# Optimization experiments

Measured on AMD Instinct MI355X. Metric: run time of the kernel, lower is better.

The kernel has to match this reference:

```python
import jax, jax.numpy as jnp
import numpy as np

NUM_GROUPS = 32
EPS = 1e-5


def _conv(x, w, b, pad):
    # x: [B,C,H,W], w: [O,I,kh,kw]
    y = jax.lax.conv_general_dilated(
        x, w, window_strides=(1, 1), padding=[(pad, pad), (pad, pad)],
        dimension_numbers=('NCHW', 'OIHW', 'NCHW'))
    return y + b[None, :, None, None]


def _group_norm(x, gamma, beta):
    B, C, H, W = x.shape
    g = x.reshape(B, NUM_GROUPS, C // NUM_GROUPS, H, W)
    mu = g.mean(axis=(2, 3, 4), keepdims=True)
    var = g.var(axis=(2, 3, 4), keepdims=True)
    g = (g - mu) * jax.lax.rsqrt(var + EPS)
    x = g.reshape(B, C, H, W)
    return x * gamma[None, :, None, None] + beta[None, :, None, None]


def setup_inputs() -> dict:
    key = jax.random.key(0)
    ks = jax.random.split(key, 8)
    B, C, H, W = 8, 384, 64, 64
    s1 = 1.0 / np.sqrt(C)          # 1x1 conv fan-in
    s3 = 1.0 / np.sqrt(C * 9)      # 3x3 conv fan-in
    return {
        'x': jax.random.normal(ks[0], (B, C, H, W), dtype=jnp.float32),
        'gamma': jnp.ones((C,), dtype=jnp.float32),
        'beta': jnp.zeros((C,), dtype=jnp.float32),
        'wq': jax.random.normal(ks[1], (C, C, 1, 1), dtype=jnp.float32) * s1,
        'bq': jnp.zeros((C,), dtype=jnp.float32),
        'wk': jax.random.normal(ks[2], (C, C, 3, 3), dtype=jnp.float32) * s3,
        'bk': jnp.zeros((C,), dtype=jnp.float32),
        'wv': jax.random.normal(ks[3], (C, C, 1, 1), dtype=jnp.float32) * s1,
        'bv': jnp.zeros((C,), dtype=jnp.float32),
        'wf': jax.random.normal(ks[4], (C, C, 1, 1), dtype=jnp.float32) * s1,
        'bf': jnp.zeros((C,), dtype=jnp.float32),
        'k': 512,
    }


def reference(x, gamma, beta, wq, bq, wk, bk, wv, bv, wf, bf, k):
    B, C, H, W = x.shape
    xn = _group_norm(x, gamma, beta)
    q = _conv(xn, wq, bq, 0)
    kk = _conv(xn, wk, bk, 1)
    v = _conv(xn, wv, bv, 0)
    # frequency-domain correlation: elementwise product of 2D spectra
    Fq = jnp.fft.fft2(q)
    Fk = jnp.fft.fft2(kk)
    A = jnp.fft.ifft2(Fq * Fk).real          # [B,C,H,W]
    # per-(batch,channel) spatial top-k sparsification
    A_flat = A.reshape(B, C, H * W)
    topv, _ = jax.lax.top_k(A_flat, k)
    thresh = topv[..., -1:]                   # k-th largest value
    masked = jnp.where(A_flat >= thresh, A_flat, -jnp.inf)
    Fw = jax.nn.softmax(masked, axis=-1).reshape(B, C, H, W)
    F4 = v * Fw                               # weighted values
    res = _conv(F4, wf, bf, 0)
    return xn * res
```

## Files before the change

### kernel.cpp

```cpp
#include <hip/hip_runtime.h>
#include <hip/hip_fp16.h>
#include <math.h>

#define CCH  384
#define BATCH 8
#define HWN  4096
#define NG   32
#define CPG  12
#define KSEL 512
#define FFTP 65
#define LP   40

typedef short v8s  __attribute__((ext_vector_type(8)));
typedef float v16f __attribute__((ext_vector_type(16)));

#define MFMA_B16(A_,B_,C_) __builtin_amdgcn_mfma_f32_32x32x16_bf16((A_),(B_),(C_),0,0,0)

#define BARRIER_NODRAIN() asm volatile("s_waitcnt lgkmcnt(0)\n\ts_barrier" ::: "memory")

__device__ __forceinline__ v8s as_v8s(uint4 u) {
  union { uint4 u4; v8s v; } c; c.u4 = u; return c.v;
}
__device__ __forceinline__ unsigned br6(unsigned i) {
  return ((i&1u)<<5)|((i&2u)<<3)|((i&4u)<<1)|((i&8u)>>1)|((i&16u)>>3)|((i&32u)>>5);
}
__device__ __forceinline__ unsigned f2key(float f) {
  unsigned u = __float_as_uint(f);
  return (u & 0x80000000u) ? ~u : (u | 0x80000000u);
}
__device__ __forceinline__ float wave_max(float v) {
#pragma unroll
  for (int o = 32; o > 0; o >>= 1) v = fmaxf(v, __shfl_down(v, o, 64));
  return v;
}
__device__ __forceinline__ float wave_sum(float v) {
#pragma unroll
  for (int o = 32; o > 0; o >>= 1) v += __shfl_down(v, o, 64);
  return v;
}
__device__ __forceinline__ unsigned short bf16_rne(float f) {
  unsigned u = __float_as_uint(f);
  return (unsigned short)((u + 0x7fffu + ((u >> 16) & 1u)) >> 16);
}
__device__ __forceinline__ float bf2f(unsigned short h) {
  return __uint_as_float(((unsigned)h) << 16);
}

__global__ __launch_bounds__(256) void stats_kernel(const float* __restrict__ x,
                                                    float2* __restrict__ gs) {
  int b = blockIdx.x >> 5, g = blockIdx.x & 31;
  size_t base = ((size_t)b * CCH + (size_t)g * CPG) * HWN;
  const float4* xp = (const float4*)(x + base);
  int tid = threadIdx.x;
  const int N4 = CPG * HWN / 4;
  float s = 0.f, ss = 0.f;
  for (int i = tid; i < N4; i += 256) {
    float4 v = xp[i];
    s  += (v.x + v.y) + (v.z + v.w);
    ss += (v.x*v.x + v.y*v.y) + (v.z*v.z + v.w*v.w);
  }
  s = wave_sum(s); ss = wave_sum(ss);
  __shared__ float sb[4], qb[4];
  if ((tid & 63) == 0) { sb[tid >> 6] = s; qb[tid >> 6] = ss; }
  __syncthreads();
  if (tid == 0) {
    float S = sb[0]+sb[1]+sb[2]+sb[3], Q = qb[0]+qb[1]+qb[2]+qb[3];
    float inv = 1.0f / (float)(CPG * HWN);
    float mu = S * inv;
    float var = Q * inv - mu * mu;
    gs[blockIdx.x] = make_float2(mu, rsqrtf(var + 1e-5f));
  }
}

__global__ __launch_bounds__(256) void pack_split_k(const float* __restrict__ w,
    unsigned short* __restrict__ hi, unsigned short* __restrict__ lo, int n) {
  int i = blockIdx.x * 256 + threadIdx.x;
  if (i >= n) return;
  float f = w[i];
  int m = i / 384, ci = i - m * 384;
  int kc = ci >> 4, tt = ci & 15;
  int mb = m >> 5, lm2 = m & 31;
  int l = ((tt >> 3) << 5) | lm2;
  int j = tt & 7;
  size_t o = (((size_t)kc * 12 + mb) << 9) + ((size_t)l << 3) + j;
  unsigned short h = bf16_rne(f);
  hi[o] = h;
  lo[o] = bf16_rne(f - bf2f(h));
}
__global__ __launch_bounds__(256) void pack9_k(const float* __restrict__ w,
    unsigned short* __restrict__ hi, unsigned short* __restrict__ lo) {
  int i = blockIdx.x * 256 + threadIdx.x;
  int r = blockIdx.y;
  float f = w[(size_t)i * 9 + r];
  int m = i / 384, ci = i - m * 384;
  int kc = ci >> 4, tt = ci & 15;
  int mb = m >> 5, lm2 = m & 31;
  int l = ((tt >> 3) << 5) | lm2;
  int j = tt & 7;
  size_t o = (((size_t)(r * 24 + kc) * 12 + mb) << 9) + ((size_t)l << 3) + j;
  unsigned short h = bf16_rne(f);
  hi[o] = h;
  lo[o] = bf16_rne(f - bf2f(h));
}

template<int FUSE, int SPLIT>
__global__ __launch_bounds__(256) void trans_kernel(const float* __restrict__ in,
    const float2* __restrict__ gs, const float* __restrict__ gamma,
    const float* __restrict__ beta,
    unsigned short* __restrict__ oh, unsigned short* __restrict__ ol) {
  __shared__ float ts[64][65];
  int tid = threadIdx.x;
  int b = blockIdx.z, c0 = blockIdx.y * 64, p0 = blockIdx.x * 64;
#pragma unroll
  for (int i = 0; i < 4; ++i) {
    int idx = tid + (i << 8);
    int row = idx >> 4, col = (idx & 15) << 2;
    float4 v = *(const float4*)&in[((size_t)b*CCH + c0 + row)*HWN + p0 + col];
    if (FUSE) {
      int c = c0 + row;
      float2 st = gs[(b << 5) + c / CPG];
      float a = gamma[c] * st.y, bb = beta[c] - st.x * a;
      v.x = v.x*a+bb; v.y = v.y*a+bb; v.z = v.z*a+bb; v.w = v.w*a+bb;
    }
    ts[row][col] = v.x; ts[row][col+1] = v.y; ts[row][col+2] = v.z; ts[row][col+3] = v.w;
  }
  __syncthreads();
#pragma unroll
  for (int i = 0; i < 2; ++i) {
    int idx = tid + (i << 8);
    int p = idx >> 3, cgp = (idx & 7) << 3;
    unsigned short h8[8] __attribute__((aligned(16)));
    unsigned short l8[8] __attribute__((aligned(16)));
#pragma unroll
    for (int j = 0; j < 8; ++j) {
      float f = ts[cgp + j][p];
      unsigned short hb = bf16_rne(f);
      h8[j] = hb;
      if (SPLIT) l8[j] = bf16_rne(f - bf2f(hb));
    }
    size_t o = ((size_t)b*HWN + p0 + p)*CCH + c0 + cgp;
    *(uint4*)&oh[o] = *(const uint4*)h8;
    if (SPLIT) *(uint4*)&ol[o] = *(const uint4*)l8;
  }
}

template<int TAPS, int OUT>
__global__ __launch_bounds__(256, 3) void mm_kernel(
    const unsigned short* __restrict__ Ahg, const unsigned short* __restrict__ Alg,
    const float* __restrict__ bias,
    const unsigned short* __restrict__ Bhg, const unsigned short* __restrict__ Blg,
    const unsigned short* __restrict__ xnTh, const unsigned short* __restrict__ xnTl,
    void* __restrict__ Yv) {
  __shared__ unsigned short Bh_s[2][128*LP], Bl_s[2][128*LP];
  int tid = threadIdx.x;
  int b = blockIdx.z, m0 = blockIdx.y * 128, n0 = blockIdx.x * 128;
  int y0 = blockIdx.x * 2;
  int u0row = tid >> 2, cg = tid & 3;
  int lds0 = u0row * LP + cg * 8, lds1 = lds0 + 64 * LP;
  int lane = tid & 63, wm = tid >> 7, wn = (tid >> 6) & 1;
  int lm = lane & 31, lh = lane >> 5;
  int brow = (wn * 64 + lm) * LP;
  int mbb = blockIdx.y * 4 + wm * 2;
  int laneoff = lane << 3;

  v16f acc[2][2];
#pragma unroll
  for (int t = 0; t < 2; ++t)
#pragma unroll
    for (int s = 0; s < 2; ++s)
#pragma unroll
      for (int g = 0; g < 16; ++g) acc[t][s][g] = 0.f;

  const int NS = TAPS * 12;
  uint4 rb0h, rb0l, rb1h, rb1l;
  uint4 rA0h_h0, rA0l_h0, rA1h_h0, rA1l_h0;
  uint4 rA0h_h1, rA0l_h1, rA1h_h1, rA1l_h1;

  auto issueB = [&](int s) {
    int r  = (TAPS == 9) ? (s / 12) : 0;
    int c0 = (s - r * 12) * 32;
    int dy = (TAPS == 9) ? r / 3 - 1 : 0;
    int dx = (TAPS == 9) ? r % 3 - 1 : 0;
    int px = u0row + dx;
    int py0 = y0 + dy, py1 = py0 + 1;
    bool okx = (unsigned)px < 64u;
    bool ok0 = okx && ((unsigned)py0 < 64u);
    bool ok1 = okx && ((unsigned)py1 < 64u);
    size_t boff0 = ((size_t)b * HWN + py0 * 64 + px) * CCH + cg * 8 + c0;
    size_t boff1 = ((size_t)b * HWN + py1 * 64 + px) * CCH + cg * 8 + c0;
    uint4 zf; zf.x = zf.y = zf.z = zf.w = 0u;
    rb0h = ok0 ? *(const uint4*)(Bhg + boff0) : zf;
    rb0l = ok0 ? *(const uint4*)(Blg + boff0) : zf;
    rb1h = ok1 ? *(const uint4*)(Bhg + boff1) : zf;
    rb1l = ok1 ? *(const uint4*)(Blg + boff1) : zf;
  };
  auto loadA0 = [&](int s) {
    int fragcol;
    if (TAPS == 9) { int r = s / 12; fragcol = r * 24 + (s - r * 12) * 2; }
    else fragcol = s * 2;
    size_t off = (((size_t)fragcol * 12 + mbb) << 9) + laneoff;
    rA0h_h0 = *(const uint4*)(Ahg + off);
    rA0l_h0 = *(const uint4*)(Alg + off);
    rA1h_h0 = *(const uint4*)(Ahg + off + 512);
    rA1l_h0 = *(const uint4*)(Alg + off + 512);
  };
  auto loadA1 = [&](int s) {
    int fragcol;
    if (TAPS == 9) { int r = s / 12; fragcol = r * 24 + (s - r * 12) * 2 + 1; }
    else fragcol = s * 2 + 1;
    size_t off = (((size_t)fragcol * 12 + mbb) << 9) + laneoff;
    rA0h_h1 = *(const uint4*)(Ahg + off);
    rA0l_h1 = *(const uint4*)(Alg + off);
    rA1h_h1 = *(const uint4*)(Ahg + off + 512);
    rA1l_h1 = *(const uint4*)(Alg + off + 512);
  };

  issueB(0);
  loadA0(0); loadA1(0);
  *(uint4*)&Bh_s[0][lds0] = rb0h; *(uint4*)&Bl_s[0][lds0] = rb0l;
  *(uint4*)&Bh_s[0][lds1] = rb1h; *(uint4*)&Bl_s[0][lds1] = rb1l;
  issueB(1);
  BARRIER_NODRAIN();

  for (int s = 0; s < NS; ++s) {
    const int cur = s & 1;
    const unsigned short* Bh = &Bh_s[cur][0];
    const unsigned short* Bl = &Bl_s[cur][0];
    {
      int co = lh << 3;
      v8s b0h = *(const v8s*)&Bh[brow + co];
      v8s b0l = *(const v8s*)&Bl[brow + co];
      v8s b1h = *(const v8s*)&Bh[brow + 32*LP + co];
      v8s b1l = *(const v8s*)&Bl[brow + 32*LP + co];
      v8s a0h = as_v8s(rA0h_h0), a0l = as_v8s(rA0l_h0);
      v8s a1h = as_v8s(rA1h_h0), a1l = as_v8s(rA1l_h0);
      __builtin_amdgcn_s_setprio(1);
      acc[0][0] = MFMA_B16(a0h, b0h, acc[0][0]);
      acc[0][0] = MFMA_B16(a0h, b0l, acc[0][0]);
      acc[0][0] = MFMA_B16(a0l, b0h, acc[0][0]);
      acc[0][1] = MFMA_B16(a0h, b1h, acc[0][1]);
      acc[0][1] = MFMA_B16(a0h, b1l, acc[0][1]);
      acc[0][1] = MFMA_B16(a0l, b1h, acc[0][1]);
      acc[1][0] = MFMA_B16(a1h, b0h, acc[1][0]);
      acc[1][0] = MFMA_B16(a1h, b0l, acc[1][0]);
      acc[1][0] = MFMA_B16(a1l, b0h, acc[1][0]);
      acc[1][1] = MFMA_B16(a1h, b1h, acc[1][1]);
      acc[1][1] = MFMA_B16(a1h, b1l, acc[1][1]);
      acc[1][1] = MFMA_B16(a1l, b1h, acc[1][1]);
      __builtin_amdgcn_s_setprio(0);
    }
    if (s + 1 < NS) loadA0(s + 1);
    {
      int co = 16 + (lh << 3);
      v8s b0h = *(const v8s*)&Bh[brow + co];
      v8s b0l = *(const v8s*)&Bl[brow + co];
      v8s b1h = *(const v8s*)&Bh[brow + 32*LP + co];
      v8s b1l = *(const v8s*)&Bl[brow + 32*LP + co];
      v8s a0h = as_v8s(rA0h_h1), a0l = as_v8s(rA0l_h1);
      v8s a1h = as_v8s(rA1h_h1), a1l = as_v8s(rA1l_h1);
      __builtin_amdgcn_s_setprio(1);
      acc[0][0] = MFMA_B16(a0h, b0h, acc[0][0]);
      acc[0][0] = MFMA_B16(a0h, b0l, acc[0][0]);
      acc[0][0] = MFMA_B16(a0l, b0h, acc[0][0]);
      acc[0][1] = MFMA_B16(a0h, b1h, acc[0][1]);
      acc[0][1] = MFMA_B16(a0h, b1l, acc[0][1]);
      acc[0][1] = MFMA_B16(a0l, b1h, acc[0][1]);
      acc[1][0] = MFMA_B16(a1h, b0h, acc[1][0]);
      acc[1][0] = MFMA_B16(a1h, b0l, acc[1][0]);
      acc[1][0] = MFMA_B16(a1l, b0h, acc[1][0]);
      acc[1][1] = MFMA_B16(a1h, b1h, acc[1][1]);
      acc[1][1] = MFMA_B16(a1h, b1l, acc[1][1]);
      acc[1][1] = MFMA_B16(a1l, b1h, acc[1][1]);
      __builtin_amdgcn_s_setprio(0);
    }
    if (s + 1 < NS) {
      loadA1(s + 1);
      int nxt = cur ^ 1;
      *(uint4*)&Bh_s[nxt][lds0] = rb0h; *(uint4*)&Bl_s[nxt][lds0] = rb0l;
      *(uint4*)&Bh_s[nxt][lds1] = rb1h; *(uint4*)&Bl_s[nxt][lds1] = rb1l;
      if (s + 2 < NS) issueB(s + 2);
      BARRIER_NODRAIN();
    }
  }
#pragma unroll
  for (int t = 0; t < 2; ++t) {
    int mb = m0 + wm * 64 + t * 32;
#pragma unroll
    for (int s = 0; s < 2; ++s) {
      int n = n0 + wn * 64 + s * 32 + lm;
#pragma unroll
      for (int g = 0; g < 16; ++g) {
        int m = mb + (g & 3) + ((g >> 2) << 3) + (lh << 2);
        float val = acc[t][s][g] + bias[m];
        size_t oidx = ((size_t)b * CCH + m) * HWN + n;
        if (OUT == 0) {
          ((float*)Yv)[oidx] = val;
        } else if (OUT == 1) {
          ((__half*)Yv)[oidx] = __float2half(val);
        } else {
          size_t tix = ((size_t)b * HWN + n) * CCH + m;
          float xnv = bf2f(xnTh[tix]) + bf2f(xnTl[tix]);
          ((float*)Yv)[oidx] = val * xnv;
        }
      }
    }
  }
}

__device__ __forceinline__ void fft4_pass(float* zr, float* zi,
    const float* twr, const float* twi, int tid, int axis, float ds) {
#pragma unroll
  for (int s = 0; s < 3; ++s) {
    const int h = 1 << (2 * s);
#pragma unroll
    for (int tt = 0; tt < 4; ++tt) {
      int t = tid + (tt << 8);
      int line = t >> 4, bf = t & 15;
      int j  = bf & (h - 1);
      int i0 = ((bf >> (2 * s)) << (2 * s + 2)) + j;
      int e1 = j << (5 - 2 * s);
      int e2 = j << (4 - 2 * s);
      float w1r = twr[e1], w1i = ds * twi[e1];
      float w2r = twr[e2], w2i = ds * twi[e2];
      int A0, st;
      if (axis == 0) { A0 = line * FFTP + i0; st = h; }
      else           { A0 = i0 * FFTP + line; st = h * FFTP; }
      int A1 = A0 + st, A2 = A1 + st, A3 = A2 + st;
      float x0r = zr[A0], x0i = zi[A0];
      float x1r = zr[A1], x1i = zi[A1];
      float x2r = zr[A2], x2i = zi[A2];
      float x3r = zr[A3], x3i = zi[A3];
      float t1r = x1r*w1r - x1i*w1i, t1i = x1r*w1i + x1i*w1r;
      float t3r = x3r*w1r - x3i*w1i, t3i = x3r*w1i + x3i*w1r;
      float u0r = x0r + t1r, u0i = x0i + t1i;
      float u1r = x0r - t1r, u1i = x0i - t1i;
      float u2r = x2r + t3r, u2i = x2i + t3i;
      float u3r = x2r - t3r, u3i = x2i - t3i;
      float c2r = u2r*w2r - u2i*w2i, c2i = u2r*w2i + u2i*w2r;
      float c3r = u3r*w2r - u3i*w2i, c3i = u3r*w2i + u3i*w2r;
      zr[A0] = u0r + c2r;      zi[A0] = u0i + c2i;
      zr[A2] = u0r - c2r;      zi[A2] = u0i - c2i;
      zr[A1] = u1r + ds*c3i;   zi[A1] = u1i - ds*c3r;
      zr[A3] = u1r - ds*c3i;   zi[A3] = u1i + ds*c3r;
    }
    __syncthreads();
  }
}

__global__ __launch_bounds__(256) void fft_topk_kernel(
    const float* q, const float* __restrict__ kkb,
    const __half* __restrict__ v, float* F4) {
  __shared__ float zr[64 * FFTP], zi[64 * FFTP];
  __shared__ float twr[32], twi[32];
  __shared__ unsigned hist[256];
  __shared__ unsigned su2[2];
  __shared__ unsigned wtot[4];
  __shared__ float sred[5];
  int tid = threadIdx.x;
  int lane = tid & 63, w = tid >> 6;
  size_t base = (size_t)blockIdx.x * HWN;
  for (int i = tid; i < HWN; i += 256) {
    int y = i >> 6, x = i & 63;
    int slot = br6(y) * FFTP + br6(x);
    zr[slot] = q[base + i];
    zi[slot] = kkb[base + i];
  }
  if (tid < 32) {
    float ang = (float)tid * 0.0981747704246810387f;
    twr[tid] = cosf(ang);
    twi[tid] = -sinf(ang);
  }
  __syncthreads();
  fft4_pass(zr, zi, twr, twi, tid, 0, 1.f);
  fft4_pass(zr, zi, twr, twi, tid, 1, 1.f);
  float prr[16], pir[16];
#pragma unroll
  for (int c = 0; c < 16; c++) {
    int i = tid + (c << 8);
    int ky = i >> 6, kx = i & 63;
    float sr = zr[ky * FFTP + kx], si = zi[ky * FFTP + kx];
    int kyn = (64 - ky) & 63, kxn = (64 - kx) & 63;
    float nr = zr[kyn * FFTP + kxn], ni = zi[kyn * FFTP + kxn];
    float fqr = 0.5f * (sr + nr), fqi = 0.5f * (si - ni);
    float fkr = 0.5f * (si + ni), fki = 0.5f * (nr - sr);
    prr[c] = fqr * fkr - fqi * fki;
    pir[c] = fqr * fki + fqi * fkr;
  }
  __syncthreads();
#pragma unroll
  for (int c = 0; c < 16; c++) {
    int i = tid + (c << 8);
    int ky = i >> 6, kx = i & 63;
    int slot = br6(ky) * FFTP + br6(kx);
    zr[slot] = prr[c];
    zi[slot] = pir[c];
  }
  __syncthreads();
  fft4_pass(zr, zi, twr, twi, tid, 0, -1.f);
  fft4_pass(zr, zi, twr, twi, tid, 1, -1.f);
  const float scale = 1.0f / 4096.0f;
  float a[16];
  unsigned key[16];
  float mx = -3.0e38f;
#pragma unroll
  for (int c = 0; c < 16; c++) {
    int i = tid + (c << 8);
    a[c] = zr[(i >> 6) * FFTP + (i & 63)] * scale;
    key[c] = f2key(a[c]);
    mx = fmaxf(mx, a[c]);
  }
  mx = wave_max(mx);
  if (lane == 0) sred[w] = mx;
  __syncthreads();
  if (tid == 0) sred[4] = fmaxf(fmaxf(sred[0], sred[1]), fmaxf(sred[2], sred[3]));
  __syncthreads();
  float am = sred[4];
  unsigned prefix = 0; int kr = KSEL;
  for (int pass = 0; pass < 4; pass++) {
    int shift = 24 - (pass << 3);
    hist[tid] = 0;
    __syncthreads();
#pragma unroll
    for (int c = 0; c < 16; c++) {
      unsigned u = key[c];
      if (((u ^ prefix) >> shift) <= 0xFFu)
        atomicAdd(&hist[(u >> shift) & 255u], 1u);
    }
    __syncthreads();
    unsigned xv = hist[tid];
#pragma unroll
    for (int o = 1; o < 64; o <<= 1) {
      unsigned t2 = __shfl_down(xv, o, 64);
      if (lane + o < 64) xv += t2;
    }
    if (lane == 0) wtot[w] = xv;
    __syncthreads();
    for (int ww = w + 1; ww < 4; ++ww) xv += wtot[ww];
    hist[tid] = xv;
    __syncthreads();
    unsigned sv = xv;
    unsigned svn = (tid < 255) ? hist[tid + 1] : 0u;
    if (sv >= (unsigned)kr && svn < (unsigned)kr) { su2[0] = (unsigned)tid; su2[1] = svn; }
    __syncthreads();
    prefix |= su2[0] << shift;
    kr -= (int)su2[1];
  }
  unsigned thr = prefix;
  float lsum = 0.f;
#pragma unroll
  for (int c = 0; c < 16; c++)
    if (key[c] >= thr) lsum += expf(a[c] - am);
  lsum = wave_sum(lsum);
  if (lane == 0) sred[w] = lsum;
  __syncthreads();
  if (tid == 0) sred[4] = 1.0f / (sred[0] + sred[1] + sred[2] + sred[3]);
  __syncthreads();
  float inv = sred[4];
#pragma unroll
  for (int c = 0; c < 16; c++) {
    int i = tid + (c << 8);
    float wgt = (key[c] >= thr) ? expf(a[c] - am) * inv : 0.f;
    F4[base + i] = __half2float(v[base + i]) * wgt;
  }
}

extern "C" void kernel_launch(void* const* d_in, const int* in_sizes, int n_in,
                              void* d_out, int out_size, void* d_ws, size_t ws_size,
                              hipStream_t stream) {
  const float* x     = (const float*)d_in[0];
  const float* gamma = (const float*)d_in[1];
  const float* beta  = (const float*)d_in[2];
  const float* wq    = (const float*)d_in[3];
  const float* bq    = (const float*)d_in[4];
  const float* wk    = (const float*)d_in[5];
  const float* bk    = (const float*)d_in[6];
  const float* wv    = (const float*)d_in[7];
  const float* bv    = (const float*)d_in[8];
  const float* wf    = (const float*)d_in[9];
  const float* bf    = (const float*)d_in[10];

  const size_t NEL = (size_t)BATCH * CCH * HWN;
  const size_t WSZ = (size_t)CCH * CCH;

  unsigned short* xnTh = (unsigned short*)d_ws;
  unsigned short* xnTl = xnTh + NEL;
  float*  qC  = (float*)(xnTl + NEL);
  float*  kD  = qC + NEL;
  __half* vE  = (__half*)(kD + NEL);
  unsigned short* W = (unsigned short*)(vE + NEL);
  unsigned short* Wqh = W;
  unsigned short* Wql = Wqh + WSZ;
  unsigned short* Wvh = Wql + WSZ;
  unsigned short* Wvl = Wvh + WSZ;
  unsigned short* Wfh = Wvl + WSZ;
  unsigned short* Wfl = Wfh + WSZ;
  unsigned short* Wkh = Wfl + WSZ;
  unsigned short* Wkl = Wkh + 9 * WSZ;
  float2* gs = (float2*)(Wkl + 9 * WSZ);
  unsigned short* F4Th = (unsigned short*)kD;
  unsigned short* F4Tl = F4Th + NEL;

  pack_split_k<<<dim3(576), dim3(256), 0, stream>>>(wq, Wqh, Wql, (int)WSZ);
  pack_split_k<<<dim3(576), dim3(256), 0, stream>>>(wv, Wvh, Wvl, (int)WSZ);
  pack_split_k<<<dim3(576), dim3(256), 0, stream>>>(wf, Wfh, Wfl, (int)WSZ);
  pack9_k<<<dim3(576, 9), dim3(256), 0, stream>>>(wk, Wkh, Wkl);
  stats_kernel<<<dim3(BATCH * NG), dim3(256), 0, stream>>>(x, gs);
  trans_kernel<1, 1><<<dim3(64, 6, BATCH), dim3(256), 0, stream>>>(
      x, gs, gamma, beta, xnTh, xnTl);

  dim3 gm(32, 3, BATCH);
  mm_kernel<1, 0><<<gm, dim3(256), 0, stream>>>(Wqh, Wql, bq, xnTh, xnTl,
                                                nullptr, nullptr, qC);
  mm_kernel<9, 0><<<gm, dim3(256), 0, stream>>>(Wkh, Wkl, bk, xnTh, xnTl,
                                                nullptr, nullptr, kD);
  mm_kernel<1, 1><<<gm, dim3(256), 0, stream>>>(Wvh, Wvl, bv, xnTh, xnTl,
                                                nullptr, nullptr, vE);

  fft_topk_kernel<<<dim3(BATCH * CCH), dim3(256), 0, stream>>>(qC, kD, vE, qC);

  trans_kernel<0, 1><<<dim3(64, 6, BATCH), dim3(256), 0, stream>>>(
      qC, nullptr, nullptr, nullptr, F4Th, F4Tl);

  mm_kernel<1, 2><<<gm, dim3(256), 0, stream>>>(Wfh, Wfl, bf, F4Th, F4Tl,
                                                xnTh, xnTl, d_out);
}
```

Baseline: 669.1 us.

## Stream GEMM B tiles directly into swizzled LDS with global_load_lds

The B operand of the bf16-split GEMM now goes straight from global memory into LDS with global_load_lds, instead of passing through registers and then being stored to LDS. The padded LDS rows are replaced by an XOR-swizzled 32-element layout to avoid bank conflicts. Out-of-bounds taps read from a small zeroed buffer, which stats_kernel clears. The main loop is reordered to one barrier per stage, independent MFMAs are interleaved, and launch bounds rise to 4 blocks per CU. This frees VGPRs and cuts LDS store traffic, but it relies on the async LDS writes being complete at a bare s_barrier with no explicit wait. It also places the zero buffer after gs, which may lie outside the allocated workspace.

```diff
diff --git a/kernel.cpp b/kernel.cpp
--- a/kernel.cpp
+++ b/kernel.cpp
@@ -9,14 +9,19 @@
 #define CPG  12
 #define KSEL 512
 #define FFTP 65
-#define LP   40
 
 typedef short v8s  __attribute__((ext_vector_type(8)));
 typedef float v16f __attribute__((ext_vector_type(16)));
 
 #define MFMA_B16(A_,B_,C_) __builtin_amdgcn_mfma_f32_32x32x16_bf16((A_),(B_),(C_),0,0,0)
 
-#define BARRIER_NODRAIN() asm volatile("s_waitcnt lgkmcnt(0)\n\ts_barrier" ::: "memory")
+#define BARRIER_RAW() asm volatile("s_barrier" ::: "memory")
+
+__device__ __forceinline__ void gl16(const unsigned short* g, unsigned short* l) {
+  __builtin_amdgcn_global_load_lds(
+      (const __attribute__((address_space(1))) unsigned int*)g,
+      (__attribute__((address_space(3))) unsigned int*)l, 16, 0, 0);
+}
 
 __device__ __forceinline__ v8s as_v8s(uint4 u) {
   union { uint4 u4; v8s v; } c; c.u4 = u; return c.v;
@@ -47,8 +52,10 @@
 }
 
 __global__ __launch_bounds__(256) void stats_kernel(const float* __restrict__ x,
-                                                    float2* __restrict__ gs) {
+                                                    float2* __restrict__ gs,
+                                                    unsigned short* __restrict__ zp) {
   int b = blockIdx.x >> 5, g = blockIdx.x & 31;
+  if (blockIdx.x == 0 && threadIdx.x < 8) zp[threadIdx.x] = 0;
   size_t base = ((size_t)b * CCH + (size_t)g * CPG) * HWN;
   const float4* xp = (const float4*)(x + base);
   int tid = threadIdx.x;
@@ -145,21 +152,19 @@
 }
 
 template<int TAPS, int OUT>
-__global__ __launch_bounds__(256, 3) void mm_kernel(
+__global__ __launch_bounds__(256, 4) void mm_kernel(
     const unsigned short* __restrict__ Ahg, const unsigned short* __restrict__ Alg,
     const float* __restrict__ bias,
     const unsigned short* __restrict__ Bhg, const unsigned short* __restrict__ Blg,
     const unsigned short* __restrict__ xnTh, const unsigned short* __restrict__ xnTl,
+    const unsigned short* __restrict__ zp,
     void* __restrict__ Yv) {
-  __shared__ unsigned short Bh_s[2][128*LP], Bl_s[2][128*LP];
+  __shared__ unsigned short Bh_s[2][4096], Bl_s[2][4096];
   int tid = threadIdx.x;
   int b = blockIdx.z, m0 = blockIdx.y * 128, n0 = blockIdx.x * 128;
   int y0 = blockIdx.x * 2;
-  int u0row = tid >> 2, cg = tid & 3;
-  int lds0 = u0row * LP + cg * 8, lds1 = lds0 + 64 * LP;
   int lane = tid & 63, wm = tid >> 7, wn = (tid >> 6) & 1;
   int lm = lane & 31, lh = lane >> 5;
-  int brow = (wn * 64 + lm) * LP;
   int mbb = blockIdx.y * 4 + wm * 2;
   int laneoff = lane << 3;
 
@@ -172,115 +177,109 @@
       for (int g = 0; g < 16; ++g) acc[t][s][g] = 0.f;
 
   const int NS = TAPS * 12;
-  uint4 rb0h, rb0l, rb1h, rb1l;
-  uint4 rA0h_h0, rA0l_h0, rA1h_h0, rA1l_h0;
-  uint4 rA0h_h1, rA0l_h1, rA1h_h1, rA1l_h1;
-
-  auto issueB = [&](int s) {
+  uint4 rA0h_0, rA0l_0, rA1h_0, rA1l_0;
+  uint4 rA0h_1, rA0l_1, rA1h_1, rA1l_1;
+
+  auto stage = [&](int s) {
+    int nxt = s & 1;
     int r  = (TAPS == 9) ? (s / 12) : 0;
     int c0 = (s - r * 12) * 32;
     int dy = (TAPS == 9) ? r / 3 - 1 : 0;
     int dx = (TAPS == 9) ? r % 3 - 1 : 0;
-    int px = u0row + dx;
-    int py0 = y0 + dy, py1 = py0 + 1;
+    int px = (tid >> 2) + dx;
     bool okx = (unsigned)px < 64u;
-    bool ok0 = okx && ((unsigned)py0 < 64u);
-    bool ok1 = okx && ((unsigned)py1 < 64u);
-    size_t boff0 = ((size_t)b * HWN + py0 * 64 + px) * CCH + cg * 8 + c0;
-    size_t boff1 = ((size_t)b * HWN + py1 * 64 + px) * CCH + cg * 8 + c0;
-    uint4 zf; zf.x = zf.y = zf.z = zf.w = 0u;
-    rb0h = ok0 ? *(const uint4*)(Bhg + boff0) : zf;
-    rb0l = ok0 ? *(const uint4*)(Blg + boff0) : zf;
-    rb1h = ok1 ? *(const uint4*)(Bhg + boff1) : zf;
-    rb1l = ok1 ? *(const uint4*)(Blg + boff1) : zf;
+    int ch = c0 + (((tid & 3) ^ ((tid >> 3) & 3)) << 3);
+    int lo = tid << 3;
+#pragma unroll
+    for (int c = 0; c < 2; ++c) {
+      int py = y0 + dy + c;
+      bool ok = okx && ((unsigned)py < 64u);
+      size_t go = ok ? (((size_t)b * HWN + py * 64 + px) * CCH + ch) : 0;
+      const unsigned short* gh = ok ? (Bhg + go) : zp;
+      const unsigned short* gl = ok ? (Blg + go) : zp;
+      gl16(gh, &Bh_s[nxt][lo + c * 2048]);
+      gl16(gl, &Bl_s[nxt][lo + c * 2048]);
+    }
   };
-  auto loadA0 = [&](int s) {
+  auto loadA_h0 = [&](int s) {
     int fragcol;
     if (TAPS == 9) { int r = s / 12; fragcol = r * 24 + (s - r * 12) * 2; }
     else fragcol = s * 2;
     size_t off = (((size_t)fragcol * 12 + mbb) << 9) + laneoff;
-    rA0h_h0 = *(const uint4*)(Ahg + off);
-    rA0l_h0 = *(const uint4*)(Alg + off);
-    rA1h_h0 = *(const uint4*)(Ahg + off + 512);
-    rA1l_h0 = *(const uint4*)(Alg + off + 512);
+    rA0h_0 = *(const uint4*)(Ahg + off);
+    rA0l_0 = *(const uint4*)(Alg + off);
+    rA1h_0 = *(const uint4*)(Ahg + off + 512);
+    rA1l_0 = *(const uint4*)(Alg + off + 512);
   };
-  auto loadA1 = [&](int s) {
+  auto loadA_h1 = [&](int s) {
     int fragcol;
     if (TAPS == 9) { int r = s / 12; fragcol = r * 24 + (s - r * 12) * 2 + 1; }
     else fragcol = s * 2 + 1;
     size_t off = (((size_t)fragcol * 12 + mbb) << 9) + laneoff;
-    rA0h_h1 = *(const uint4*)(Ahg + off);
-    rA0l_h1 = *(const uint4*)(Alg + off);
-    rA1h_h1 = *(const uint4*)(Ahg + off + 512);
-    rA1l_h1 = *(const uint4*)(Alg + off + 512);
+    rA0h_1 = *(const uint4*)(Ahg + off);
+    rA0l_1 = *(const uint4*)(Alg + off);
+    rA1h_1 = *(const uint4*)(Ahg + off + 512);
+    rA1l_1 = *(const uint4*)(Alg + off + 512);
   };
-
-  issueB(0);
-  loadA0(0); loadA1(0);
-  *(uint4*)&Bh_s[0][lds0] = rb0h; *(uint4*)&Bl_s[0][lds0] = rb0l;
-  *(uint4*)&Bh_s[0][lds1] = rb1h; *(uint4*)&Bl_s[0][lds1] = rb1l;
-  issueB(1);
-  BARRIER_NODRAIN();
+  auto ldB = [&](const unsigned short* base, int sb, int slot) -> v8s {
+    int row = wn * 64 + sb * 32 + lm;
+    int se = slot ^ ((row >> 1) & 3);
+    return *(const v8s*)&base[row * 32 + (se << 3)];
+  };
+
+  stage(0);
+  __builtin_amdgcn_sched_barrier(0);
+  loadA_h0(0);
+  __syncthreads();
 
   for (int s = 0; s < NS; ++s) {
-    const int cur = s & 1;
-    const unsigned short* Bh = &Bh_s[cur][0];
-    const unsigned short* Bl = &Bl_s[cur][0];
+    const unsigned short* Bhc = &Bh_s[s & 1][0];
+    const unsigned short* Blc = &Bl_s[s & 1][0];
+    if (s + 1 < NS) stage(s + 1);
+    __builtin_amdgcn_sched_barrier(0);
+    loadA_h1(s);
     {
-      int co = lh << 3;
-      v8s b0h = *(const v8s*)&Bh[brow + co];
-      v8s b0l = *(const v8s*)&Bl[brow + co];
-      v8s b1h = *(const v8s*)&Bh[brow + 32*LP + co];
-      v8s b1l = *(const v8s*)&Bl[brow + 32*LP + co];
-      v8s a0h = as_v8s(rA0h_h0), a0l = as_v8s(rA0l_h0);
-      v8s a1h = as_v8s(rA1h_h0), a1l = as_v8s(rA1l_h0);
+      v8s b0h = ldB(Bhc, 0, lh),     b1h = ldB(Bhc, 1, lh);
+      v8s b0l = ldB(Blc, 0, lh),     b1l = ldB(Blc, 1, lh);
+      v8s a0h = as_v8s(rA0h_0), a0l = as_v8s(rA0l_0);
+      v8s a1h = as_v8s(rA1h_0), a1l = as_v8s(rA1l_0);
       __builtin_amdgcn_s_setprio(1);
       acc[0][0] = MFMA_B16(a0h, b0h, acc[0][0]);
+      acc[0][1] = MFMA_B16(a0h, b1h, acc[0][1]);
+      acc[1][0] = MFMA_B16(a1h, b0h, acc[1][0]);
+      acc[1][1] = MFMA_B16(a1h, b1h, acc[1][1]);
       acc[0][0] = MFMA_B16(a0h, b0l, acc[0][0]);
+      acc[0][1] = MFMA_B16(a0h, b1l, acc[0][1]);
+      acc[1][0] = MFMA_B16(a1h, b0l, acc[1][0]);
+      acc[1][1] = MFMA_B16(a1h, b1l, acc[1][1]);
       acc[0][0] = MFMA_B16(a0l, b0h, acc[0][0]);
-      acc[0][1] = MFMA_B16(a0h, b1h, acc[0][1]);
-      acc[0][1] = MFMA_B16(a0h, b1l, acc[0][1]);
       acc[0][1] = MFMA_B16(a0l, b1h, acc[0][1]);
-      acc[1][0] = MFMA_B16(a1h, b0h, acc[1][0]);
-      acc[1][0] = MFMA_B16(a1h, b0l, acc[1][0]);
       acc[1][0] = MFMA_B16(a1l, b0h, acc[1][0]);
-      acc[1][1] = MFMA_B16(a1h, b1h, acc[1][1]);
-      acc[1][1] = MFMA_B16(a1h, b1l, acc[1][1]);
       acc[1][1] = MFMA_B16(a1l, b1h, acc[1][1]);
       __builtin_amdgcn_s_setprio(0);
     }
-    if (s + 1 < NS) loadA0(s + 1);
+    if (s + 1 < NS) loadA_h0(s + 1);
     {
-      int co = 16 + (lh << 3);
-      v8s b0h = *(const v8s*)&Bh[brow + co];
-      v8s b0l = *(const v8s*)&Bl[brow + co];
-      v8s b1h = *(const v8s*)&Bh[brow + 32*LP + co];
-      v8s b1l = *(const v8s*)&Bl[brow + 32*LP + co];
-      v8s a0h = as_v8s(rA0h_h1), a0l = as_v8s(rA0l_h1);
-      v8s a1h = as_v8s(rA1h_h1), a1l = as_v8s(rA1l_h1);
+      v8s b0h = ldB(Bhc, 0, 2 + lh), b1h = ldB(Bhc, 1, 2 + lh);
+      v8s b0l = ldB(Blc, 0, 2 + lh), b1l = ldB(Blc, 1, 2 + lh);
+      v8s a0h = as_v8s(rA0h_1), a0l = as_v8s(rA0l_1);
+      v8s a1h = as_v8s(rA1h_1), a1l = as_v8s(rA1l_1);
       __builtin_amdgcn_s_setprio(1);
       acc[0][0] = MFMA_B16(a0h, b0h, acc[0][0]);
+      acc[0][1] = MFMA_B16(a0h, b1h, acc[0][1]);
+      acc[1][0] = MFMA_B16(a1h, b0h, acc[1][0]);
+      acc[1][1] = MFMA_B16(a1h, b1h, acc[1][1]);
       acc[0][0] = MFMA_B16(a0h, b0l, acc[0][0]);
+      acc[0][1] = MFMA_B16(a0h, b1l, acc[0][1]);
+      acc[1][0] = MFMA_B16(a1h, b0l, acc[1][0]);
+      acc[1][1] = MFMA_B16(a1h, b1l, acc[1][1]);
       acc[0][0] = MFMA_B16(a0l, b0h, acc[0][0]);
-      acc[0][1] = MFMA_B16(a0h, b1h, acc[0][1]);
-      acc[0][1] = MFMA_B16(a0h, b1l, acc[0][1]);
       acc[0][1] = MFMA_B16(a0l, b1h, acc[0][1]);
-      acc[1][0] = MFMA_B16(a1h, b0h, acc[1][0]);
-      acc[1][0] = MFMA_B16(a1h, b0l, acc[1][0]);
       acc[1][0] = MFMA_B16(a1l, b0h, acc[1][0]);
-      acc[1][1] = MFMA_B16(a1h, b1h, acc[1][1]);
-      acc[1][1] = MFMA_B16(a1h, b1l, acc[1][1]);
       acc[1][1] = MFMA_B16(a1l, b1h, acc[1][1]);
       __builtin_amdgcn_s_setprio(0);
     }
-    if (s + 1 < NS) {
-      loadA1(s + 1);
-      int nxt = cur ^ 1;
-      *(uint4*)&Bh_s[nxt][lds0] = rb0h; *(uint4*)&Bl_s[nxt][lds0] = rb0l;
-      *(uint4*)&Bh_s[nxt][lds1] = rb1h; *(uint4*)&Bl_s[nxt][lds1] = rb1l;
-      if (s + 2 < NS) issueB(s + 2);
-      BARRIER_NODRAIN();
-    }
+    BARRIER_RAW();
   }
 #pragma unroll
   for (int t = 0; t < 2; ++t) {
@@ -497,6 +496,7 @@
   unsigned short* Wkh = Wfl + WSZ;
   unsigned short* Wkl = Wkh + 9 * WSZ;
   float2* gs = (float2*)(Wkl + 9 * WSZ);
+  unsigned short* zp = (unsigned short*)(gs + BATCH * NG);
   unsigned short* F4Th = (unsigned short*)kD;
   unsigned short* F4Tl = F4Th + NEL;
 
@@ -504,17 +504,17 @@
   pack_split_k<<<dim3(576), dim3(256), 0, stream>>>(wv, Wvh, Wvl, (int)WSZ);
   pack_split_k<<<dim3(576), dim3(256), 0, stream>>>(wf, Wfh, Wfl, (int)WSZ);
   pack9_k<<<dim3(576, 9), dim3(256), 0, stream>>>(wk, Wkh, Wkl);
-  stats_kernel<<<dim3(BATCH * NG), dim3(256), 0, stream>>>(x, gs);
+  stats_kernel<<<dim3(BATCH * NG), dim3(256), 0, stream>>>(x, gs, zp);
   trans_kernel<1, 1><<<dim3(64, 6, BATCH), dim3(256), 0, stream>>>(
       x, gs, gamma, beta, xnTh, xnTl);
 
   dim3 gm(32, 3, BATCH);
   mm_kernel<1, 0><<<gm, dim3(256), 0, stream>>>(Wqh, Wql, bq, xnTh, xnTl,
-                                                nullptr, nullptr, qC);
+                                                nullptr, nullptr, zp, qC);
   mm_kernel<9, 0><<<gm, dim3(256), 0, stream>>>(Wkh, Wkl, bk, xnTh, xnTl,
-                                                nullptr, nullptr, kD);
+                                                nullptr, nullptr, zp, kD);
   mm_kernel<1, 1><<<gm, dim3(256), 0, stream>>>(Wvh, Wvl, bv, xnTh, xnTl,
-                                                nullptr, nullptr, vE);
+                                                nullptr, nullptr, zp, vE);
 
   fft_topk_kernel<<<dim3(BATCH * CCH), dim3(256), 0, stream>>>(qC, kD, vE, qC);
 
@@ -522,5 +522,5 @@
       qC, nullptr, nullptr, nullptr, F4Th, F4Tl);
 
   mm_kernel<1, 2><<<gm, dim3(256), 0, stream>>>(Wfh, Wfl, bf, F4Th, F4Tl,
-                                                xnTh, xnTl, d_out);
-}
+                                                xnTh, xnTl, zp, d_out);
+}
```

Measured after the change: 730.6 us. +9.2%, slower.

## Add dedicated 3x3 conv kernel reusing haloed LDS slab across horizontal taps

Applied to the files above, without the earlier changes.

Adds a dedicated kernel for the 3x3 key convolution. For each dy row and channel chunk it stages one two-row input slab with zero halo columns into LDS, then reuses that slab for all three dx taps. The generic kernel is simplified to 1x1 only. Before, each tap reloaded B from global memory with bounds checks. Out-of-range rows now read from a zeroed scratch buffer instead of taking a branch. Separately, the top-k radix histogram is split into one copy per wave to reduce LDS atomic contention. The cost is more LDS use and extra barriers.

```diff
diff --git a/kernel.cpp b/kernel.cpp
--- a/kernel.cpp
+++ b/kernel.cpp
@@ -17,6 +17,7 @@
 #define MFMA_B16(A_,B_,C_) __builtin_amdgcn_mfma_f32_32x32x16_bf16((A_),(B_),(C_),0,0,0)
 
 #define BARRIER_NODRAIN() asm volatile("s_waitcnt lgkmcnt(0)\n\ts_barrier" ::: "memory")
+#define BARRIER_RAW() asm volatile("s_barrier" ::: "memory")
 
 __device__ __forceinline__ v8s as_v8s(uint4 u) {
   union { uint4 u4; v8s v; } c; c.u4 = u; return c.v;
@@ -47,8 +48,10 @@
 }
 
 __global__ __launch_bounds__(256) void stats_kernel(const float* __restrict__ x,
-                                                    float2* __restrict__ gs) {
+                                                    float2* __restrict__ gs,
+                                                    unsigned short* __restrict__ zp) {
   int b = blockIdx.x >> 5, g = blockIdx.x & 31;
+  if (blockIdx.x == 0 && threadIdx.x < 8) zp[threadIdx.x] = 0;
   size_t base = ((size_t)b * CCH + (size_t)g * CPG) * HWN;
   const float4* xp = (const float4*)(x + base);
   int tid = threadIdx.x;
@@ -177,27 +180,18 @@
   uint4 rA0h_h1, rA0l_h1, rA1h_h1, rA1l_h1;
 
   auto issueB = [&](int s) {
-    int r  = (TAPS == 9) ? (s / 12) : 0;
-    int c0 = (s - r * 12) * 32;
-    int dy = (TAPS == 9) ? r / 3 - 1 : 0;
-    int dx = (TAPS == 9) ? r % 3 - 1 : 0;
-    int px = u0row + dx;
-    int py0 = y0 + dy, py1 = py0 + 1;
-    bool okx = (unsigned)px < 64u;
-    bool ok0 = okx && ((unsigned)py0 < 64u);
-    bool ok1 = okx && ((unsigned)py1 < 64u);
+    int c0 = s * 32;
+    int px = u0row;
+    int py0 = y0, py1 = py0 + 1;
     size_t boff0 = ((size_t)b * HWN + py0 * 64 + px) * CCH + cg * 8 + c0;
     size_t boff1 = ((size_t)b * HWN + py1 * 64 + px) * CCH + cg * 8 + c0;
-    uint4 zf; zf.x = zf.y = zf.z = zf.w = 0u;
-    rb0h = ok0 ? *(const uint4*)(Bhg + boff0) : zf;
-    rb0l = ok0 ? *(const uint4*)(Blg + boff0) : zf;
-    rb1h = ok1 ? *(const uint4*)(Bhg + boff1) : zf;
-    rb1l = ok1 ? *(const uint4*)(Blg + boff1) : zf;
+    rb0h = *(const uint4*)(Bhg + boff0);
+    rb0l = *(const uint4*)(Blg + boff0);
+    rb1h = *(const uint4*)(Bhg + boff1);
+    rb1l = *(const uint4*)(Blg + boff1);
   };
   auto loadA0 = [&](int s) {
-    int fragcol;
-    if (TAPS == 9) { int r = s / 12; fragcol = r * 24 + (s - r * 12) * 2; }
-    else fragcol = s * 2;
+    int fragcol = s * 2;
     size_t off = (((size_t)fragcol * 12 + mbb) << 9) + laneoff;
     rA0h_h0 = *(const uint4*)(Ahg + off);
     rA0l_h0 = *(const uint4*)(Alg + off);
@@ -205,9 +199,7 @@
     rA1l_h0 = *(const uint4*)(Alg + off + 512);
   };
   auto loadA1 = [&](int s) {
-    int fragcol;
-    if (TAPS == 9) { int r = s / 12; fragcol = r * 24 + (s - r * 12) * 2 + 1; }
-    else fragcol = s * 2 + 1;
+    int fragcol = s * 2 + 1;
     size_t off = (((size_t)fragcol * 12 + mbb) << 9) + laneoff;
     rA0h_h1 = *(const uint4*)(Ahg + off);
     rA0l_h1 = *(const uint4*)(Alg + off);
@@ -302,6 +294,182 @@
           float xnv = bf2f(xnTh[tix]) + bf2f(xnTl[tix]);
           ((float*)Yv)[oidx] = val * xnv;
         }
+      }
+    }
+  }
+}
+
+__global__ __launch_bounds__(256, 3) void mm9_kernel(
+    const unsigned short* __restrict__ Ahg, const unsigned short* __restrict__ Alg,
+    const float* __restrict__ bias,
+    const unsigned short* __restrict__ Bhg, const unsigned short* __restrict__ Blg,
+    const unsigned short* __restrict__ zp,
+    float* __restrict__ Y) {
+  __shared__ unsigned short Bh_s[2*66*LP], Bl_s[2*66*LP];
+  int tid = threadIdx.x;
+  int b = blockIdx.z, m0 = blockIdx.y * 128, n0 = blockIdx.x * 128;
+  int y0 = blockIdx.x * 2;
+  int lane = tid & 63, wm = tid >> 7, wn = (tid >> 6) & 1;
+  int lm = lane & 31, lh = lane >> 5;
+  int mbb = blockIdx.y * 4 + wm * 2;
+  int laneoff = lane << 3;
+
+  v16f acc[2][2];
+#pragma unroll
+  for (int t = 0; t < 2; ++t)
+#pragma unroll
+    for (int s = 0; s < 2; ++s)
+#pragma unroll
+      for (int g = 0; g < 16; ++g) acc[t][s][g] = 0.f;
+
+  if (tid < 128) {
+    int py = (tid >> 6) & 1, e = (tid >> 5) & 1, ch = tid & 31;
+    int px = e ? 65 : 0;
+    Bh_s[(py*66 + px)*LP + ch] = 0;
+    Bl_s[(py*66 + px)*LP + ch] = 0;
+  }
+
+  uint4 rs0, rs1, rs2, rs3;
+  auto issueSlab = [&](int si2) {
+    int dyi2 = si2 / 12, cidx2 = si2 - dyi2 * 12;
+    int dy = dyi2 - 1;
+    int r2 = tid & 255;
+    int py0c = (tid >> 8);
+    (void)py0c;
+#pragma unroll
+    for (int k2 = 0; k2 < 4; ++k2) {
+      int cid = tid + (k2 << 8);
+      int rr = cid & 511;
+      int py = rr >> 8;
+      int r3 = rr & 255;
+      int px0 = r3 >> 2, cs = r3 & 3;
+      int pyi = y0 + dy + py;
+      bool ok = (unsigned)pyi < 64u;
+      size_t go = ok ? (((size_t)b * HWN + pyi * 64 + px0) * CCH + cidx2 * 32 + cs * 8) : 0;
+      const unsigned short* src = (cid < 512) ? (ok ? Bhg + go : zp)
+                                              : (ok ? Blg + go : zp);
+      uint4 v = *(const uint4*)src;
+      if (k2 == 0) rs0 = v; else if (k2 == 1) rs1 = v;
+      else if (k2 == 2) rs2 = v; else rs3 = v;
+    }
+    (void)r2;
+  };
+  auto writeSlab = [&]() {
+#pragma unroll
+    for (int k2 = 0; k2 < 4; ++k2) {
+      int cid = tid + (k2 << 8);
+      int rr = cid & 511;
+      int py = rr >> 8;
+      int r3 = rr & 255;
+      int px0 = r3 >> 2, cs = r3 & 3;
+      int dst = (py * 66 + px0 + 1) * LP + cs * 8;
+      unsigned short* arr = (cid < 512) ? Bh_s : Bl_s;
+      uint4 v = (k2 == 0) ? rs0 : (k2 == 1) ? rs1 : (k2 == 2) ? rs2 : rs3;
+      *(uint4*)&arr[dst] = v;
+    }
+  };
+
+  uint4 rA0h_h0, rA0l_h0, rA1h_h0, rA1l_h0;
+  uint4 rA0h_h1, rA0l_h1, rA1h_h1, rA1l_h1;
+  auto loadAh0 = [&](int fragcol) {
+    size_t off = (((size_t)fragcol * 12 + mbb) << 9) + laneoff;
+    rA0h_h0 = *(const uint4*)(Ahg + off);
+    rA0l_h0 = *(const uint4*)(Alg + off);
+    rA1h_h0 = *(const uint4*)(Ahg + off + 512);
+    rA1l_h0 = *(const uint4*)(Alg + off + 512);
+  };
+  auto loadAh1 = [&](int fragcol) {
+    size_t off = (((size_t)(fragcol + 1) * 12 + mbb) << 9) + laneoff;
+    rA0h_h1 = *(const uint4*)(Ahg + off);
+    rA0l_h1 = *(const uint4*)(Alg + off);
+    rA1h_h1 = *(const uint4*)(Ahg + off + 512);
+    rA1l_h1 = *(const uint4*)(Alg + off + 512);
+  };
+  auto ldS = [&](const unsigned short* base, int sb, int h, int dx) -> v8s {
+    int px = sb * 32 + lm + dx + 1;
+    return *(const v8s*)&base[(wn * 66 + px) * LP + h * 16 + lh * 8];
+  };
+
+  issueSlab(0);
+  writeSlab();
+  issueSlab(1);
+  loadAh0(0);
+  loadAh1(0);
+  __syncthreads();
+
+  int dyi = 0, cidx = 0;
+  for (int si = 0; si < 36; ++si) {
+    int rbase = dyi * 3;
+    int ndyi = (cidx == 11) ? dyi + 1 : dyi;
+    int ncidx = (cidx == 11) ? 0 : cidx + 1;
+#pragma unroll
+    for (int dxi = 0; dxi < 3; ++dxi) {
+      const int dx = dxi - 1;
+      bool last = (si == 35) && (dxi == 2);
+      int nfc = (dxi < 2) ? ((rbase + dxi + 1) * 24 + cidx * 2)
+                          : ((ndyi * 3) * 24 + ncidx * 2);
+      {
+        v8s b0h = ldS(Bh_s, 0, 0, dx), b1h = ldS(Bh_s, 1, 0, dx);
+        v8s b0l = ldS(Bl_s, 0, 0, dx), b1l = ldS(Bl_s, 1, 0, dx);
+        v8s a0h = as_v8s(rA0h_h0), a0l = as_v8s(rA0l_h0);
+        v8s a1h = as_v8s(rA1h_h0), a1l = as_v8s(rA1l_h0);
+        __builtin_amdgcn_s_setprio(1);
+        acc[0][0] = MFMA_B16(a0h, b0h, acc[0][0]);
+        acc[0][0] = MFMA_B16(a0h, b0l, acc[0][0]);
+        acc[0][0] = MFMA_B16(a0l, b0h, acc[0][0]);
+        acc[0][1] = MFMA_B16(a0h, b1h, acc[0][1]);
+        acc[0][1] = MFMA_B16(a0h, b1l, acc[0][1]);
+        acc[0][1] = MFMA_B16(a0l, b1h, acc[0][1]);
+        acc[1][0] = MFMA_B16(a1h, b0h, acc[1][0]);
+        acc[1][0] = MFMA_B16(a1h, b0l, acc[1][0]);
+        acc[1][0] = MFMA_B16(a1l, b0h, acc[1][0]);
+        acc[1][1] = MFMA_B16(a1h, b1h, acc[1][1]);
+        acc[1][1] = MFMA_B16(a1h, b1l, acc[1][1]);
+        acc[1][1] = MFMA_B16(a1l, b1h, acc[1][1]);
+        __builtin_amdgcn_s_setprio(0);
+      }
+      if (!last) loadAh0(nfc);
+      {
+        v8s b0h = ldS(Bh_s, 0, 1, dx), b1h = ldS(Bh_s, 1, 1, dx);
+        v8s b0l = ldS(Bl_s, 0, 1, dx), b1l = ldS(Bl_s, 1, 1, dx);
+        v8s a0h = as_v8s(rA0h_h1), a0l = as_v8s(rA0l_h1);
+        v8s a1h = as_v8s(rA1h_h1), a1l = as_v8s(rA1l_h1);
+        __builtin_amdgcn_s_setprio(1);
+        acc[0][0] = MFMA_B16(a0h, b0h, acc[0][0]);
+        acc[0][0] = MFMA_B16(a0h, b0l, acc[0][0]);
+        acc[0][0] = MFMA_B16(a0l, b0h, acc[0][0]);
+        acc[0][1] = MFMA_B16(a0h, b1h, acc[0][1]);
+        acc[0][1] = MFMA_B16(a0h, b1l, acc[0][1]);
+        acc[0][1] = MFMA_B16(a0l, b1h, acc[0][1]);
+        acc[1][0] = MFMA_B16(a1h, b0h, acc[1][0]);
+        acc[1][0] = MFMA_B16(a1h, b0l, acc[1][0]);
+        acc[1][0] = MFMA_B16(a1l, b0h, acc[1][0]);
+        acc[1][1] = MFMA_B16(a1h, b1h, acc[1][1]);
+        acc[1][1] = MFMA_B16(a1h, b1l, acc[1][1]);
+        acc[1][1] = MFMA_B16(a1l, b1h, acc[1][1]);
+        __builtin_amdgcn_s_setprio(0);
+      }
+      if (!last) loadAh1(nfc);
+    }
+    if (si < 35) {
+      BARRIER_RAW();
+      writeSlab();
+      if (si + 2 < 36) issueSlab(si + 2);
+      BARRIER_NODRAIN();
+    }
+    dyi = ndyi; cidx = ncidx;
+  }
+
+#pragma unroll
+  for (int t = 0; t < 2; ++t) {
+    int mb = m0 + wm * 64 + t * 32;
+#pragma unroll
+    for (int s = 0; s < 2; ++s) {
+      int n = n0 + wn * 64 + s * 32 + lm;
+#pragma unroll
+      for (int g = 0; g < 16; ++g) {
+        int m = mb + (g & 3) + ((g >> 2) << 3) + (lh << 2);
+        Y[((size_t)b * CCH + m) * HWN + n] = acc[t][s][g] + bias[m];
       }
     }
   }
@@ -352,7 +520,7 @@
     const __half* __restrict__ v, float* F4) {
   __shared__ float zr[64 * FFTP], zi[64 * FFTP];
   __shared__ float twr[32], twi[32];
-  __shared__ unsigned hist[256];
+  __shared__ unsigned hist[4][256];
   __shared__ unsigned su2[2];
   __shared__ unsigned wtot[4];
   __shared__ float sred[5];
@@ -418,16 +586,17 @@
   unsigned prefix = 0; int kr = KSEL;
   for (int pass = 0; pass < 4; pass++) {
     int shift = 24 - (pass << 3);
-    hist[tid] = 0;
+#pragma unroll
+    for (int ww = 0; ww < 4; ++ww) hist[ww][tid] = 0;
     __syncthreads();
 #pragma unroll
     for (int c = 0; c < 16; c++) {
       unsigned u = key[c];
       if (((u ^ prefix) >> shift) <= 0xFFu)
-        atomicAdd(&hist[(u >> shift) & 255u], 1u);
+        atomicAdd(&hist[w][(u >> shift) & 255u], 1u);
     }
     __syncthreads();
-    unsigned xv = hist[tid];
+    unsigned xv = hist[0][tid] + hist[1][tid] + hist[2][tid] + hist[3][tid];
 #pragma unroll
     for (int o = 1; o < 64; o <<= 1) {
       unsigned t2 = __shfl_down(xv, o, 64);
@@ -436,10 +605,10 @@
     if (lane == 0) wtot[w] = xv;
     __syncthreads();
     for (int ww = w + 1; ww < 4; ++ww) xv += wtot[ww];
-    hist[tid] = xv;
+    hist[0][tid] = xv;
     __syncthreads();
     unsigned sv = xv;
-    unsigned svn = (tid < 255) ? hist[tid + 1] : 0u;
+    unsigned svn = (tid < 255) ? hist[0][tid + 1] : 0u;
     if (sv >= (unsigned)kr && svn < (unsigned)kr) { su2[0] = (unsigned)tid; su2[1] = svn; }
     __syncthreads();
     prefix |= su2[0] << shift;
@@ -497,6 +666,7 @@
   unsigned short* Wkh = Wfl + WSZ;
   unsigned short* Wkl = Wkh + 9 * WSZ;
   float2* gs = (float2*)(Wkl + 9 * WSZ);
+  unsigned short* zp = (unsigned short*)(gs + BATCH * NG);
   unsigned short* F4Th = (unsigned short*)kD;
   unsigned short* F4Tl = F4Th + NEL;
 
@@ -504,15 +674,14 @@
   pack_split_k<<<dim3(576), dim3(256), 0, stream>>>(wv, Wvh, Wvl, (int)WSZ);
   pack_split_k<<<dim3(576), dim3(256), 0, stream>>>(wf, Wfh, Wfl, (int)WSZ);
   pack9_k<<<dim3(576, 9), dim3(256), 0, stream>>>(wk, Wkh, Wkl);
-  stats_kernel<<<dim3(BATCH * NG), dim3(256), 0, stream>>>(x, gs);
+  stats_kernel<<<dim3(BATCH * NG), dim3(256), 0, stream>>>(x, gs, zp);
   trans_kernel<1, 1><<<dim3(64, 6, BATCH), dim3(256), 0, stream>>>(
       x, gs, gamma, beta, xnTh, xnTl);
 
   dim3 gm(32, 3, BATCH);
   mm_kernel<1, 0><<<gm, dim3(256), 0, stream>>>(Wqh, Wql, bq, xnTh, xnTl,
                                                 nullptr, nullptr, qC);
-  mm_kernel<9, 0><<<gm, dim3(256), 0, stream>>>(Wkh, Wkl, bk, xnTh, xnTl,
-                                                nullptr, nullptr, kD);
+  mm9_kernel<<<gm, dim3(256), 0, stream>>>(Wkh, Wkl, bk, xnTh, xnTl, zp, kD);
   mm_kernel<1, 1><<<gm, dim3(256), 0, stream>>>(Wvh, Wvl, bv, xnTh, xnTl,
                                                 nullptr, nullptr, vE);
 
```

Result: faster. 641.5 us (-4.1%).
